# Kernel optimization log

Hardware: AMD Instinct MI355X
Metric: run time of the kernel (lower is better)

The kernel has to match this reference:

```python
import jax, jax.numpy as jnp
import numpy as np

B, C, H, W = 16, 256, 32, 32
LN_EPS = 1e-5


def setup_inputs() -> dict:
    key = jax.random.key(0)
    ks = jax.random.split(key, 12)
    s = 1.0 / np.sqrt(C)
    x = jax.random.normal(ks[0], (B, C, H, W), dtype=jnp.float32)
    # Linear weights stored as [in, out] (torch stores [out, in]; math is x @ W_in_out + b)
    wq = jax.random.uniform(ks[1], (C, C), jnp.float32, -s, s)
    bq = jax.random.uniform(ks[2], (C,), jnp.float32, -s, s)
    wk = jax.random.uniform(ks[3], (C, C), jnp.float32, -s, s)
    bk = jax.random.uniform(ks[4], (C,), jnp.float32, -s, s)
    wv = jax.random.uniform(ks[5], (C, C), jnp.float32, -s, s)
    bv = jax.random.uniform(ks[6], (C,), jnp.float32, -s, s)
    w1 = jax.random.uniform(ks[7], (C, C), jnp.float32, -s, s)
    b1 = jax.random.uniform(ks[8], (C,), jnp.float32, -s, s)
    w2 = jax.random.uniform(ks[9], (C, C), jnp.float32, -s, s)
    b2 = jax.random.uniform(ks[10], (C,), jnp.float32, -s, s)
    gamma = jnp.ones((C,), jnp.float32)
    beta = jnp.zeros((C,), jnp.float32)
    return {"x": x, "wq": wq, "bq": bq, "wk": wk, "bk": bk, "wv": wv, "bv": bv,
            "w1": w1, "b1": b1, "w2": w2, "b2": b2, "gamma": gamma, "beta": beta}


def reference(x, wq, bq, wk, bk, wv, bv, w1, b1, w2, b2, gamma, beta):
    Bd, Cd, Hd, Wd = x.shape
    t = x.reshape(Bd, Cd, Hd * Wd).transpose(0, 2, 1)  # [B, N, C]
    q = t @ wq + bq
    k = t @ wk + bk
    v = t @ wv + bv
    # matrix[b,i,j] = q[b,i,:] . k[b,j,:]  (no 1/sqrt(d) scaling, as in source)
    m = jnp.einsum('bic,bjc->bij', q, k)
    # softmax over dim=-2 (the query axis i)
    m = jax.nn.softmax(m, axis=-2)
    # att[b,j,c] = sum_i v[b,i,c] * m[b,i,j]  (v^T @ m, then permute)
    att = jnp.einsum('bic,bij->bjc', v, m)  # [B, N, C]
    # MLP (SiLU, hidden = C), dropout p=0 -> identity; DropPath eval -> identity
    att = jax.nn.silu(att @ w1 + b1) @ w2 + b2
    # LayerNorm over channel dim
    mu = jnp.mean(att, axis=-1, keepdims=True)
    var = jnp.var(att, axis=-1, keepdims=True)
    att = (att - mu) * jax.lax.rsqrt(var + LN_EPS) * gamma + beta
    return att.transpose(0, 2, 1).reshape(Bd, Cd, Hd, Wd)
```

## Files before the change

kernel.cpp:

```cpp
#include <hip/hip_runtime.h>

#define BB 16
#define CC 256
#define NN 1024

typedef _Float16 f16;
typedef __attribute__((ext_vector_type(8))) _Float16 half8;
typedef __attribute__((ext_vector_type(4))) float f32x4;

__device__ __forceinline__ half8 ldg8(const f16* p) {
  return *reinterpret_cast<const half8*>(p);
}

__device__ __forceinline__ void gll16(const f16* g, f16* l) {
  __builtin_amdgcn_global_load_lds((const __attribute__((address_space(1))) void*)g,
                                   (__attribute__((address_space(3))) void*)l, 16, 0, 0);
}

#define VMCNT(n) asm volatile("s_waitcnt vmcnt(" #n ")" ::: "memory")
#define BAR() __builtin_amdgcn_s_barrier()

__device__ __forceinline__ void stage32k8(const f16* __restrict__ g, f16* l, int wave, int lane) {
#pragma unroll
  for (int k = 0; k < 4; ++k) {
    int ob = k * 4096 + wave * 512;
    gll16(g + ob + lane * 8, l + ob);
  }
}

struct WP5 {
  const float* s[5];
  f16* d[5];
};

__global__ void __launch_bounds__(256) k_packW(WP5 p) {
  __shared__ float ws[256][17];
  int m = blockIdx.y, ct = blockIdx.x;
  const float* W = p.s[m];
  f16* wp = p.d[m];
  int tid = threadIdx.x;
  int col = tid & 15, cig = tid >> 4;
#pragma unroll
  for (int pg = 0; pg < 16; ++pg) {
    int ci = pg * 16 + cig;
    ws[ci][col] = W[(size_t)ci * 256 + ct * 16 + col];
  }
  __syncthreads();
  int lane = tid & 63, wave = tid >> 6;
  int row16 = lane & 15, quad = lane >> 4;
#pragma unroll
  for (int kk = 0; kk < 2; ++kk) {
    int kc = wave * 2 + kk;
    half8 o;
#pragma unroll
    for (int j = 0; j < 8; ++j) o[j] = (f16)ws[kc * 32 + quad * 8 + j][row16];
    *reinterpret_cast<half8*>(wp + ((size_t)ct * 8 + kc) * 512 + lane * 8) = o;
  }
}

struct QkvSmem {
  union {
    struct { f16 hi[32][264]; f16 lo[32][264]; } ts;
    f16 ex[2][16][264];
    f16 exv[256][40];
  };
};

__global__ void __launch_bounds__(256, 2) k_qkv(const float* __restrict__ x,
    const f16* __restrict__ wqp, const f16* __restrict__ wkp, const f16* __restrict__ wvp,
    const float* __restrict__ bq, const float* __restrict__ bk, const float* __restrict__ bv,
    f16* __restrict__ qp, f16* __restrict__ kp, f16* __restrict__ vp, int b_base) {
  __shared__ QkvSmem sm;
  int bl = blockIdx.x, bg = b_base + bl, n0 = blockIdx.y * 32;
  int tid = threadIdx.x, wave = tid >> 6, lane = tid & 63;
  int row16 = lane & 15, quad = lane >> 4;
  int g = wave >> 1, h = wave & 1;

#pragma unroll
  for (int e = tid; e < 2048; e += 256) {
    int c = e >> 3, n4 = (e & 7) << 2;
    float4 u = *reinterpret_cast<const float4*>(x + (size_t)(bg * CC + c) * NN + n0 + n4);
    float uv[4] = {u.x, u.y, u.z, u.w};
#pragma unroll
    for (int i = 0; i < 4; ++i) {
      f16 hh = (f16)uv[i];
      sm.ts.hi[n4 + i][c] = hh;
      sm.ts.lo[n4 + i][c] = (f16)(uv[i] - (float)hh);
    }
  }
  __syncthreads();

  half8 ah[8], al[8];
#pragma unroll
  for (int kc = 0; kc < 8; ++kc) {
    ah[kc] = *reinterpret_cast<const half8*>(&sm.ts.hi[g * 16 + row16][kc * 32 + quad * 8]);
    al[kc] = *reinterpret_cast<const half8*>(&sm.ts.lo[g * 16 + row16][kc * 32 + quad * 8]);
  }
  __syncthreads();

  const f16* WTs[2]    = {wqp, wkp};
  const float* biases[2] = {bq, bk};
  f16* outs[2]         = {qp, kp};
#pragma unroll
  for (int z = 0; z < 2; ++z) {
    const f16* WT = WTs[z];
    const float* bias = biases[z];
    f16* outp = outs[z];
#pragma unroll
    for (int cp = 0; cp < 2; ++cp) {
      f32x4 acch[4], accl[4];
#pragma unroll
      for (int u = 0; u < 4; ++u) { acch[u] = {0.f,0.f,0.f,0.f}; accl[u] = {0.f,0.f,0.f,0.f}; }
#pragma unroll
      for (int kc = 0; kc < 8; ++kc) {
#pragma unroll
        for (int u = 0; u < 4; ++u) {
          int ct = h * 8 + cp * 4 + u;
          half8 b = ldg8(WT + ((size_t)ct * 8 + kc) * 512 + lane * 8);
          acch[u] = __builtin_amdgcn_mfma_f32_16x16x32_f16(ah[kc], b, acch[u], 0, 0, 0);
          accl[u] = __builtin_amdgcn_mfma_f32_16x16x32_f16(al[kc], b, accl[u], 0, 0, 0);
        }
      }
#pragma unroll
      for (int u = 0; u < 4; ++u) {
        int ct = h * 8 + cp * 4 + u;
        int co = ct * 16 + row16;
        float bb = bias[co];
#pragma unroll
        for (int r = 0; r < 4; ++r)
          sm.ex[g][quad * 4 + r][co] = (f16)(acch[u][r] + accl[u][r] + bb);
      }
    }
    const f16* exr = &sm.ex[g][row16][0];
    size_t fb = ((size_t)bl * 64 + (n0 >> 4) + g) * 8;
#pragma unroll
    for (int k = 0; k < 4; ++k) {
      int kc = h * 4 + k;
      half8 hv = *reinterpret_cast<const half8*>(exr + kc * 32 + quad * 8);
      *reinterpret_cast<half8*>(outp + (fb + kc) * 512 + lane * 8) = hv;
    }
  }
  __syncthreads();

#pragma unroll
  for (int cp = 0; cp < 2; ++cp) {
    f32x4 acch[4], accl[4];
#pragma unroll
    for (int u = 0; u < 4; ++u) { acch[u] = {0.f,0.f,0.f,0.f}; accl[u] = {0.f,0.f,0.f,0.f}; }
#pragma unroll
    for (int kc = 0; kc < 8; ++kc) {
#pragma unroll
      for (int u = 0; u < 4; ++u) {
        int ct = h * 8 + cp * 4 + u;
        half8 b = ldg8(wvp + ((size_t)ct * 8 + kc) * 512 + lane * 8);
        acch[u] = __builtin_amdgcn_mfma_f32_16x16x32_f16(ah[kc], b, acch[u], 0, 0, 0);
        accl[u] = __builtin_amdgcn_mfma_f32_16x16x32_f16(al[kc], b, accl[u], 0, 0, 0);
      }
    }
#pragma unroll
    for (int u = 0; u < 4; ++u) {
      int ct = h * 8 + cp * 4 + u;
      int co = ct * 16 + row16;
      float bb = bv[co];
#pragma unroll
      for (int r = 0; r < 4; ++r)
        sm.exv[co][g * 16 + quad * 4 + r] = (f16)(acch[u][r] + accl[u][r] + bb);
    }
  }
  __syncthreads();
  size_t vb = ((size_t)bl * 32 + blockIdx.y) * 16;
#pragma unroll
  for (int f = 0; f < 4; ++f) {
    int ct = wave * 4 + f;
    half8 o = *reinterpret_cast<const half8*>(&sm.exv[ct * 16 + row16][quad * 8]);
    *reinterpret_cast<half8*>(vp + (vb + ct) * 512 + lane * 8) = o;
  }
}

struct AttnSmem {
  union {
    struct {
      f16 QB[2][64 * 256];
      f16 VB[2][64 * 256];
    } s;
    struct {
      float Ocmb[4][16][260];
      f16 ex[4][16][264];
    } e;
  } u;
  f16 P[8][16][40];
  float ml[8][2][16];
  float lnbuf[8][2][16];
};

__global__ void __launch_bounds__(512, 2) k_attn_mlp(
    const f16* __restrict__ qp, const f16* __restrict__ kp, const f16* __restrict__ vp,
    const f16* __restrict__ w1p, const float* __restrict__ b1,
    const f16* __restrict__ w2p, const float* __restrict__ b2,
    const float* __restrict__ gamma, const float* __restrict__ beta,
    float* __restrict__ out, int b_base) {
  __shared__ AttnSmem sm;
  int bl = blockIdx.x, bg = b_base + bl;
  int j0 = blockIdx.y * 64;
  int tid = threadIdx.x, wave = tid >> 6, lane = tid & 63;
  int row16 = lane & 15, quad = lane >> 4;
  int jt_l = wave & 3, p = wave >> 2;
  int jw = j0 + jt_l * 16;

  const f16* kbase = kp + (size_t)bl * NN * CC;
  int jt = (j0 >> 4) + jt_l;
  half8 kf[8];
#pragma unroll
  for (int kc = 0; kc < 8; ++kc)
    kf[kc] = ldg8(kbase + ((size_t)jt * 8 + kc) * 512 + lane * 8);

  const f16* qbase = qp + (size_t)bl * NN * CC;
  const f16* vbase = vp + (size_t)bl * CC * NN;

  stage32k8(qbase, sm.u.s.QB[0], wave, lane);
  stage32k8(vbase, sm.u.s.VB[0], wave, lane);
  VMCNT(0);
  BAR();

  f32x4 O[16];
#pragma unroll
  for (int ct = 0; ct < 16; ++ct) O[ct] = {0.f, 0.f, 0.f, 0.f};
  float m_run[4], l_lane[4];
#pragma unroll
  for (int r = 0; r < 4; ++r) { m_run[r] = -1e30f; l_lane[r] = 0.f; }

  int cur = 0;
  for (int it = 0; it < 16; ++it) {
    const f16* QBp = &sm.u.s.QB[cur][p * 8192];
    const f16* VBp = &sm.u.s.VB[cur][p * 8192];

    stage32k8(qbase + (size_t)((it + 1) & 15) * 16384, sm.u.s.QB[cur ^ 1], wave, lane);
    stage32k8(vbase + (size_t)((it + 1) & 15) * 16384, sm.u.s.VB[cur ^ 1], wave, lane);

    f32x4 s[2];
#pragma unroll
    for (int f = 0; f < 2; ++f) s[f] = {0.f, 0.f, 0.f, 0.f};
#pragma unroll
    for (int kc = 0; kc < 8; ++kc) {
#pragma unroll
      for (int f = 0; f < 2; ++f) {
        half8 b = *reinterpret_cast<const half8*>(&QBp[(f * 8 + kc) * 512 + lane * 8]);
        s[f] = __builtin_amdgcn_mfma_f32_16x16x32_f16(kf[kc], b, s[f], 0, 0, 0);
      }
    }

    float alpha[4];
#pragma unroll
    for (int r = 0; r < 4; ++r) {
      float mx = fmaxf(s[0][r], s[1][r]);
#pragma unroll
      for (int off = 1; off < 16; off <<= 1) mx = fmaxf(mx, __shfl_xor(mx, off, 64));
      float mnew = fmaxf(m_run[r], mx);
      alpha[r] = __expf(m_run[r] - mnew);
      m_run[r] = mnew;
      float ps = 0.f;
#pragma unroll
      for (int f = 0; f < 2; ++f) {
        float pv = __expf(s[f][r] - mnew);
        ps += pv;
        sm.P[wave][quad * 4 + r][f * 16 + row16] = (f16)pv;
      }
      l_lane[r] = l_lane[r] * alpha[r] + ps;
    }
#pragma unroll
    for (int ct = 0; ct < 16; ++ct)
#pragma unroll
      for (int r = 0; r < 4; ++r) O[ct][r] *= alpha[r];

    {
      half8 pf = *reinterpret_cast<const half8*>(&sm.P[wave][row16][quad * 8]);
#pragma unroll
      for (int ct = 0; ct < 16; ++ct) {
        half8 vf = *reinterpret_cast<const half8*>(&VBp[ct * 512 + lane * 8]);
        O[ct] = __builtin_amdgcn_mfma_f32_16x16x32_f16(pf, vf, O[ct], 0, 0, 0);
      }
    }

    VMCNT(0);
    BAR();
    cur ^= 1;
  }

#pragma unroll
  for (int r = 0; r < 4; ++r) {
#pragma unroll
    for (int off = 1; off < 16; off <<= 1) l_lane[r] += __shfl_xor(l_lane[r], off, 64);
  }
  if (row16 == 0) {
#pragma unroll
    for (int r = 0; r < 4; ++r) {
      sm.ml[wave][0][quad * 4 + r] = m_run[r];
      sm.ml[wave][1][quad * 4 + r] = l_lane[r];
    }
  }
  BAR();

  int partner = wave ^ 4;
  float aS[4], invL[4];
#pragma unroll
  for (int r = 0; r < 4; ++r) {
    int j = quad * 4 + r;
    float ma = m_run[r], mb = sm.ml[partner][0][j];
    float M = fmaxf(ma, mb);
    float L = l_lane[r] * __expf(ma - M) + sm.ml[partner][1][j] * __expf(mb - M);
    aS[r] = __expf(ma - M);
    invL[r] = 1.f / L;
  }
#pragma unroll
  for (int ct = 0; ct < 16; ++ct)
#pragma unroll
    for (int r = 0; r < 4; ++r) O[ct][r] *= aS[r];

  if (p == 1) {
#pragma unroll
    for (int ct = 0; ct < 16; ++ct)
#pragma unroll
      for (int r = 0; r < 4; ++r)
        sm.u.e.Ocmb[jt_l][quad * 4 + r][ct * 16 + row16] = O[ct][r];
  }
  BAR();
  if (p == 0) {
#pragma unroll
    for (int ct = 0; ct < 16; ++ct)
#pragma unroll
      for (int r = 0; r < 4; ++r) {
        float v = sm.u.e.Ocmb[jt_l][quad * 4 + r][ct * 16 + row16] + O[ct][r];
        sm.u.e.ex[jt_l][quad * 4 + r][ct * 16 + row16] = (f16)(v * invL[r]);
      }
  }
  BAR();

  half8 af[8];
#pragma unroll
  for (int kc = 0; kc < 8; ++kc)
    af[kc] = *reinterpret_cast<const half8*>(&sm.u.e.ex[jt_l][row16][kc * 32 + quad * 8]);

  f16* ex2 = reinterpret_cast<f16*>(&sm.u.e.Ocmb[0][0][0]);

#pragma unroll
  for (int q8 = 0; q8 < 8; ++q8) {
    int ct = p * 8 + q8;
    f32x4 acc = {0.f, 0.f, 0.f, 0.f};
    const f16* brow = w1p + ((size_t)ct * 8) * 512 + lane * 8;
#pragma unroll
    for (int kc = 0; kc < 8; ++kc)
      acc = __builtin_amdgcn_mfma_f32_16x16x32_f16(af[kc], ldg8(brow + kc * 512), acc, 0, 0, 0);
    int co = ct * 16 + row16;
    float bb = b1[co];
#pragma unroll
    for (int r = 0; r < 4; ++r) {
      float xg = acc[r] + bb;
      float hh = xg / (1.f + __expf(-xg));
      ex2[((size_t)jt_l * 16 + quad * 4 + r) * 264 + co] = (f16)hh;
    }
  }
  BAR();

  half8 hf[8];
#pragma unroll
  for (int kc = 0; kc < 8; ++kc)
    hf[kc] = *reinterpret_cast<const half8*>(&ex2[((size_t)jt_l * 16 + row16) * 264 + kc * 32 + quad * 8]);

  f32x4 acc2[8];
#pragma unroll
  for (int q8 = 0; q8 < 8; ++q8) {
    int ct = p * 8 + q8;
    f32x4 acc = {0.f, 0.f, 0.f, 0.f};
    const f16* brow = w2p + ((size_t)ct * 8) * 512 + lane * 8;
#pragma unroll
    for (int kc = 0; kc < 8; ++kc)
      acc = __builtin_amdgcn_mfma_f32_16x16x32_f16(hf[kc], ldg8(brow + kc * 512), acc, 0, 0, 0);
    float bb = b2[ct * 16 + row16];
#pragma unroll
    for (int r = 0; r < 4; ++r) acc[r] += bb;
    acc2[q8] = acc;
  }

  float sum[4] = {0.f, 0.f, 0.f, 0.f}, ssq[4] = {0.f, 0.f, 0.f, 0.f};
#pragma unroll
  for (int q8 = 0; q8 < 8; ++q8)
#pragma unroll
    for (int r = 0; r < 4; ++r) { float xv = acc2[q8][r]; sum[r] += xv; ssq[r] += xv * xv; }
#pragma unroll
  for (int r = 0; r < 4; ++r) {
#pragma unroll
    for (int off = 1; off < 16; off <<= 1) {
      sum[r] += __shfl_xor(sum[r], off, 64);
      ssq[r] += __shfl_xor(ssq[r], off, 64);
    }
  }
  if (row16 == 0) {
#pragma unroll
    for (int r = 0; r < 4; ++r) {
      sm.lnbuf[wave][0][quad * 4 + r] = sum[r];
      sm.lnbuf[wave][1][quad * 4 + r] = ssq[r];
    }
  }
  BAR();

  float mean[4], rstd[4];
#pragma unroll
  for (int r = 0; r < 4; ++r) {
    int j = quad * 4 + r;
    float s  = sm.lnbuf[wave][0][j] + sm.lnbuf[partner][0][j];
    float sq = sm.lnbuf[wave][1][j] + sm.lnbuf[partner][1][j];
    mean[r] = s * (1.f / 256.f);
    float var = sq * (1.f / 256.f) - mean[r] * mean[r];
    rstd[r] = rsqrtf(var + 1e-5f);
  }

#pragma unroll
  for (int q8 = 0; q8 < 8; ++q8) {
    int col = (p * 8 + q8) * 16 + row16;
    float g = gamma[col], be = beta[col];
    f32x4 v;
#pragma unroll
    for (int r = 0; r < 4; ++r) v[r] = (acc2[q8][r] - mean[r]) * rstd[r] * g + be;
    *reinterpret_cast<f32x4*>(out + (size_t)(bg * CC + col) * NN + jw + quad * 4) = v;
  }
}

extern "C" void kernel_launch(void* const* d_in, const int* in_sizes, int n_in,
                              void* d_out, int out_size, void* d_ws, size_t ws_size,
                              hipStream_t stream) {
  (void)in_sizes; (void)n_in; (void)out_size;
  const float* x     = (const float*)d_in[0];
  const float* wq    = (const float*)d_in[1];
  const float* bq    = (const float*)d_in[2];
  const float* wk    = (const float*)d_in[3];
  const float* bk    = (const float*)d_in[4];
  const float* wv    = (const float*)d_in[5];
  const float* bv    = (const float*)d_in[6];
  const float* w1    = (const float*)d_in[7];
  const float* b1    = (const float*)d_in[8];
  const float* w2    = (const float*)d_in[9];
  const float* b2    = (const float*)d_in[10];
  const float* gamma = (const float*)d_in[11];
  const float* beta  = (const float*)d_in[12];
  float* out = (float*)d_out;

  const size_t WE = 65536;
  const size_t SB = (size_t)NN * CC;
  f16* base = (f16*)d_ws;
  f16* wqp = base + 0 * WE;
  f16* wkp = base + 1 * WE;
  f16* wvp = base + 2 * WE;
  f16* w1p = base + 3 * WE;
  f16* w2p = base + 4 * WE;

  size_t wbytes = 5 * WE * sizeof(f16);
  size_t perb   = 3 * SB * sizeof(f16);
  int nb = (ws_size > wbytes) ? (int)((ws_size - wbytes) / perb) : 1;
  if (nb < 1) nb = 1;
  if (nb > BB) nb = BB;

  f16* qb  = base + 5 * WE;
  f16* kb  = qb + (size_t)nb * SB;
  f16* vTb = kb + (size_t)nb * SB;

  WP5 p;
  p.s[0] = wq; p.s[1] = wk; p.s[2] = wv; p.s[3] = w1; p.s[4] = w2;
  p.d[0] = wqp; p.d[1] = wkp; p.d[2] = wvp; p.d[3] = w1p; p.d[4] = w2p;
  k_packW<<<dim3(16, 5), 256, 0, stream>>>(p);

  for (int b0 = 0; b0 < BB; b0 += nb) {
    int cb = (b0 + nb <= BB) ? nb : (BB - b0);
    k_qkv<<<dim3(cb, 32), 256, 0, stream>>>(x, wqp, wkp, wvp, bq, bk, bv, qb, kb, vTb, b0);
    k_attn_mlp<<<dim3(cb, 16), 512, 0, stream>>>(qb, kb, vTb, w1p, b1, w2p, b2,
                                                 gamma, beta, out, b0);
  }
}
```

Measured before the change: 194.1 us.

## Split QKV projection across grid z and skip redundant softmax rescaling

```diff
diff --git a/kernel.cpp b/kernel.cpp
--- a/kernel.cpp
+++ b/kernel.cpp
@@ -66,11 +66,12 @@
   };
 };
 
-__global__ void __launch_bounds__(256, 2) k_qkv(const float* __restrict__ x,
+__global__ void __launch_bounds__(256, 4) k_qkv(const float* __restrict__ x,
     const f16* __restrict__ wqp, const f16* __restrict__ wkp, const f16* __restrict__ wvp,
     const float* __restrict__ bq, const float* __restrict__ bk, const float* __restrict__ bv,
     f16* __restrict__ qp, f16* __restrict__ kp, f16* __restrict__ vp, int b_base) {
   __shared__ QkvSmem sm;
+  int z = blockIdx.z;
   int bl = blockIdx.x, bg = b_base + bl, n0 = blockIdx.y * 32;
   int tid = threadIdx.x, wave = tid >> 6, lane = tid & 63;
   int row16 = lane & 15, quad = lane >> 4;
@@ -98,82 +99,89 @@
   }
   __syncthreads();
 
-  const f16* WTs[2]    = {wqp, wkp};
-  const float* biases[2] = {bq, bk};
-  f16* outs[2]         = {qp, kp};
-#pragma unroll
-  for (int z = 0; z < 2; ++z) {
-    const f16* WT = WTs[z];
-    const float* bias = biases[z];
-    f16* outp = outs[z];
+  if (z == 0) {
+    const f16* WTs[2]      = {wqp, wkp};
+    const float* biases[2] = {bq, bk};
+    f16* outs[2]           = {qp, kp};
+#pragma unroll
+    for (int zz = 0; zz < 2; ++zz) {
+      const f16* WT = WTs[zz];
+      const float* bias = biases[zz];
+      f16* outp = outs[zz];
+#pragma unroll
+      for (int cp = 0; cp < 2; ++cp) {
+#pragma unroll
+        for (int uu = 0; uu < 2; ++uu) {
+          f32x4 acch[2], accl[2];
+#pragma unroll
+          for (int u = 0; u < 2; ++u) { acch[u] = {0.f,0.f,0.f,0.f}; accl[u] = {0.f,0.f,0.f,0.f}; }
+#pragma unroll
+          for (int kc = 0; kc < 8; ++kc) {
+#pragma unroll
+            for (int u = 0; u < 2; ++u) {
+              int ct = h * 8 + cp * 4 + uu * 2 + u;
+              half8 b = ldg8(WT + ((size_t)ct * 8 + kc) * 512 + lane * 8);
+              acch[u] = __builtin_amdgcn_mfma_f32_16x16x32_f16(ah[kc], b, acch[u], 0, 0, 0);
+              accl[u] = __builtin_amdgcn_mfma_f32_16x16x32_f16(al[kc], b, accl[u], 0, 0, 0);
+            }
+          }
+#pragma unroll
+          for (int u = 0; u < 2; ++u) {
+            int ct = h * 8 + cp * 4 + uu * 2 + u;
+            int co = ct * 16 + row16;
+            float bb = bias[co];
+#pragma unroll
+            for (int r = 0; r < 4; ++r)
+              sm.ex[g][quad * 4 + r][co] = (f16)(acch[u][r] + accl[u][r] + bb);
+          }
+        }
+      }
+      const f16* exr = &sm.ex[g][row16][0];
+      size_t fb = ((size_t)bl * 64 + (n0 >> 4) + g) * 8;
+#pragma unroll
+      for (int k = 0; k < 4; ++k) {
+        int kc = h * 4 + k;
+        half8 hv = *reinterpret_cast<const half8*>(exr + kc * 32 + quad * 8);
+        *reinterpret_cast<half8*>(outp + (fb + kc) * 512 + lane * 8) = hv;
+      }
+    }
+  } else {
 #pragma unroll
     for (int cp = 0; cp < 2; ++cp) {
-      f32x4 acch[4], accl[4];
-#pragma unroll
-      for (int u = 0; u < 4; ++u) { acch[u] = {0.f,0.f,0.f,0.f}; accl[u] = {0.f,0.f,0.f,0.f}; }
-#pragma unroll
-      for (int kc = 0; kc < 8; ++kc) {
-#pragma unroll
-        for (int u = 0; u < 4; ++u) {
-          int ct = h * 8 + cp * 4 + u;
-          half8 b = ldg8(WT + ((size_t)ct * 8 + kc) * 512 + lane * 8);
-          acch[u] = __builtin_amdgcn_mfma_f32_16x16x32_f16(ah[kc], b, acch[u], 0, 0, 0);
-          accl[u] = __builtin_amdgcn_mfma_f32_16x16x32_f16(al[kc], b, accl[u], 0, 0, 0);
+#pragma unroll
+      for (int uu = 0; uu < 2; ++uu) {
+        f32x4 acch[2], accl[2];
+#pragma unroll
+        for (int u = 0; u < 2; ++u) { acch[u] = {0.f,0.f,0.f,0.f}; accl[u] = {0.f,0.f,0.f,0.f}; }
+#pragma unroll
+        for (int kc = 0; kc < 8; ++kc) {
+#pragma unroll
+          for (int u = 0; u < 2; ++u) {
+            int ct = h * 8 + cp * 4 + uu * 2 + u;
+            half8 b = ldg8(wvp + ((size_t)ct * 8 + kc) * 512 + lane * 8);
+            acch[u] = __builtin_amdgcn_mfma_f32_16x16x32_f16(ah[kc], b, acch[u], 0, 0, 0);
+            accl[u] = __builtin_amdgcn_mfma_f32_16x16x32_f16(al[kc], b, accl[u], 0, 0, 0);
+          }
         }
-      }
-#pragma unroll
-      for (int u = 0; u < 4; ++u) {
-        int ct = h * 8 + cp * 4 + u;
-        int co = ct * 16 + row16;
-        float bb = bias[co];
-#pragma unroll
-        for (int r = 0; r < 4; ++r)
-          sm.ex[g][quad * 4 + r][co] = (f16)(acch[u][r] + accl[u][r] + bb);
-      }
-    }
-    const f16* exr = &sm.ex[g][row16][0];
-    size_t fb = ((size_t)bl * 64 + (n0 >> 4) + g) * 8;
-#pragma unroll
-    for (int k = 0; k < 4; ++k) {
-      int kc = h * 4 + k;
-      half8 hv = *reinterpret_cast<const half8*>(exr + kc * 32 + quad * 8);
-      *reinterpret_cast<half8*>(outp + (fb + kc) * 512 + lane * 8) = hv;
-    }
-  }
-  __syncthreads();
-
-#pragma unroll
-  for (int cp = 0; cp < 2; ++cp) {
-    f32x4 acch[4], accl[4];
-#pragma unroll
-    for (int u = 0; u < 4; ++u) { acch[u] = {0.f,0.f,0.f,0.f}; accl[u] = {0.f,0.f,0.f,0.f}; }
-#pragma unroll
-    for (int kc = 0; kc < 8; ++kc) {
-#pragma unroll
-      for (int u = 0; u < 4; ++u) {
-        int ct = h * 8 + cp * 4 + u;
-        half8 b = ldg8(wvp + ((size_t)ct * 8 + kc) * 512 + lane * 8);
-        acch[u] = __builtin_amdgcn_mfma_f32_16x16x32_f16(ah[kc], b, acch[u], 0, 0, 0);
-        accl[u] = __builtin_amdgcn_mfma_f32_16x16x32_f16(al[kc], b, accl[u], 0, 0, 0);
-      }
-    }
-#pragma unroll
-    for (int u = 0; u < 4; ++u) {
-      int ct = h * 8 + cp * 4 + u;
-      int co = ct * 16 + row16;
-      float bb = bv[co];
-#pragma unroll
-      for (int r = 0; r < 4; ++r)
-        sm.exv[co][g * 16 + quad * 4 + r] = (f16)(acch[u][r] + accl[u][r] + bb);
-    }
-  }
-  __syncthreads();
-  size_t vb = ((size_t)bl * 32 + blockIdx.y) * 16;
-#pragma unroll
-  for (int f = 0; f < 4; ++f) {
-    int ct = wave * 4 + f;
-    half8 o = *reinterpret_cast<const half8*>(&sm.exv[ct * 16 + row16][quad * 8]);
-    *reinterpret_cast<half8*>(vp + (vb + ct) * 512 + lane * 8) = o;
+#pragma unroll
+        for (int u = 0; u < 2; ++u) {
+          int ct = h * 8 + cp * 4 + uu * 2 + u;
+          int co = ct * 16 + row16;
+          float bb = bv[co];
+#pragma unroll
+          for (int r = 0; r < 4; ++r)
+            sm.exv[co][g * 16 + quad * 4 + r] = (f16)(acch[u][r] + accl[u][r] + bb);
+        }
+      }
+    }
+    __syncthreads();
+    size_t vb = ((size_t)bl * 32 + blockIdx.y) * 16;
+#pragma unroll
+    for (int f = 0; f < 4; ++f) {
+      int ct = wave * 4 + f;
+      half8 o = *reinterpret_cast<const half8*>(&sm.exv[ct * 16 + row16][quad * 8]);
+      *reinterpret_cast<half8*>(vp + (vb + ct) * 512 + lane * 8) = o;
+    }
   }
 }
 
@@ -249,28 +257,41 @@
       }
     }
 
-    float alpha[4];
+    float mx4[4];
+    bool need = false;
 #pragma unroll
     for (int r = 0; r < 4; ++r) {
       float mx = fmaxf(s[0][r], s[1][r]);
 #pragma unroll
       for (int off = 1; off < 16; off <<= 1) mx = fmaxf(mx, __shfl_xor(mx, off, 64));
-      float mnew = fmaxf(m_run[r], mx);
-      alpha[r] = __expf(m_run[r] - mnew);
-      m_run[r] = mnew;
+      mx4[r] = mx;
+      need = need || (mx > m_run[r]);
+    }
+    if (__any(need)) {
+      float alpha[4];
+#pragma unroll
+      for (int r = 0; r < 4; ++r) {
+        float mnew = fmaxf(m_run[r], mx4[r]);
+        alpha[r] = __expf(m_run[r] - mnew);
+        m_run[r] = mnew;
+        l_lane[r] *= alpha[r];
+      }
+#pragma unroll
+      for (int ct = 0; ct < 16; ++ct)
+#pragma unroll
+        for (int r = 0; r < 4; ++r) O[ct][r] *= alpha[r];
+    }
+#pragma unroll
+    for (int r = 0; r < 4; ++r) {
       float ps = 0.f;
 #pragma unroll
       for (int f = 0; f < 2; ++f) {
-        float pv = __expf(s[f][r] - mnew);
+        float pv = __expf(s[f][r] - m_run[r]);
         ps += pv;
         sm.P[wave][quad * 4 + r][f * 16 + row16] = (f16)pv;
       }
-      l_lane[r] = l_lane[r] * alpha[r] + ps;
-    }
-#pragma unroll
-    for (int ct = 0; ct < 16; ++ct)
-#pragma unroll
-      for (int r = 0; r < 4; ++r) O[ct][r] *= alpha[r];
+      l_lane[r] += ps;
+    }
 
     {
       half8 pf = *reinterpret_cast<const half8*>(&sm.P[wave][row16][quad * 8]);
@@ -470,7 +491,7 @@
 
   for (int b0 = 0; b0 < BB; b0 += nb) {
     int cb = (b0 + nb <= BB) ? nb : (BB - b0);
-    k_qkv<<<dim3(cb, 32), 256, 0, stream>>>(x, wqp, wkp, wvp, bq, bk, bv, qb, kb, vTb, b0);
+    k_qkv<<<dim3(cb, 32, 2), 256, 0, stream>>>(x, wqp, wkp, wvp, bq, bk, bv, qb, kb, vTb, b0);
     k_attn_mlp<<<dim3(cb, 16), 512, 0, stream>>>(qb, kb, vTb, w1p, b1, w2p, b2,
                                                  gamma, beta, out, b0);
   }
```

New measurement: 187.0 us. 1.04x faster.
